# Kernel optimization log

Measured on AMD Instinct MI355X. Metric: run time of the kernel, lower is better.

The kernel has to match this reference:

```python
import jax, jax.numpy as jnp
import numpy as np

D_MODEL = 1024
NUM_EXPERTS = 16
TOP_K = 2
TOP_C = 4  # min(E, max(4, 2*top_k))
TAU = 1.0
RANK = 64  # max(4, d_model // 16)


def _stable_softmax(v):
    m = jnp.max(v, axis=-1, keepdims=True)
    e = jnp.exp(v - m)
    return e / (jnp.sum(e, axis=-1, keepdims=True) + 1e-12)


def setup_inputs() -> dict:
    key = jax.random.key(0)
    ks = jax.random.split(key, 8)
    B, D, E, R = 16384, D_MODEL, NUM_EXPERTS, RANK
    x = jax.random.normal(ks[0], (B, D), dtype=jnp.float32)
    W_enc = jax.random.normal(ks[1], (D, D), dtype=jnp.float32) * (1.0 / np.sqrt(D))
    b_enc = jnp.zeros((D,), dtype=jnp.float32)
    W_gate = jax.random.normal(ks[2], (E, D), dtype=jnp.float32) * (1.0 / np.sqrt(D))
    U = jax.random.normal(ks[3], (E, R, D), dtype=jnp.float32) * (1.0 / np.sqrt(D))
    V = jax.random.normal(ks[4], (E, D, R), dtype=jnp.float32) * (1.0 / np.sqrt(R))
    gamma = jnp.ones((E,), dtype=jnp.float32)
    return {"x": x, "W_enc": W_enc, "b_enc": b_enc, "W_gate": W_gate,
            "U": U, "V": V, "gamma": gamma}


def reference(x, W_enc, b_enc, W_gate, U, V, gamma):
    # shared encoder
    encoded = x @ W_enc.T + b_enc                      # [B, D]
    # gating: logits -> top_c -> top_k -> softmax over selected logits
    logits = (encoded @ W_gate.T) / TAU                # [B, E]
    topc_vals, topc_idx = jax.lax.top_k(logits, TOP_C)
    topk_vals, pos_in_c = jax.lax.top_k(topc_vals, TOP_K)
    topk_idx = jnp.take_along_axis(topc_idx, pos_in_c, axis=1)  # [B, K]
    topk_w = _stable_softmax(topk_vals)                # [B, K], all > 1e-12
    # dense per-(token, expert) combine weight (equivalent to gather/scatter)
    B = x.shape[0]
    w_dense = jnp.zeros((B, NUM_EXPERTS), dtype=x.dtype)
    w_dense = w_dense.at[jnp.arange(B)[:, None], topk_idx].add(topk_w)
    # low-rank experts: delta_e(x) = gamma_e * silu(x U_e^T) V_e^T
    s = jax.nn.silu(jnp.einsum('bd,erd->ber', encoded, U))        # [B, E, R]
    coef = w_dense * gamma[None, :]                               # [B, E]
    delta = jnp.einsum('ber,edr->bd', s * coef[..., None], V)     # [B, D]
    # y = encoded + sum_k w_k * (expert(x) - x)  with expert(x)-x = delta_e
    return encoded + delta
```

## Files before the change

kernel.cpp:

```cpp
#include <hip/hip_runtime.h>
#include <hip/hip_bf16.h>

#define D_DIM 1024
#define NE 16
#define RK 64
#define NTOK 16384

typedef __bf16 bf16;
typedef __bf16 bf16x8 __attribute__((ext_vector_type(8)));
typedef __bf16 bf16x4 __attribute__((ext_vector_type(4)));
typedef float f32x4 __attribute__((ext_vector_type(4)));

__device__ __forceinline__ void gload16(const void* g, void* l) {
  __builtin_amdgcn_global_load_lds((const __attribute__((address_space(1))) unsigned int*)g,
                                   (__attribute__((address_space(3))) unsigned int*)l,
                                   16, 0, 0);
}

__global__ void k_cast(const float* __restrict__ s, bf16* __restrict__ d, int n4) {
  int i = blockIdx.x * blockDim.x + threadIdx.x;
  if (i >= n4) return;
  float4 v = ((const float4*)s)[i];
  bf16x4 o = { (bf16)v.x, (bf16)v.y, (bf16)v.z, (bf16)v.w };
  ((bf16x4*)d)[i] = o;
}

__global__ void k_castv(const float* __restrict__ V, bf16* __restrict__ Vb2) {
  int id = blockIdx.x * 256 + threadIdx.x;
  int d = id & 1023;
  int rb = (id >> 10) & 7;
  int e = id >> 13;
  const float* src = V + ((size_t)(e * 1024 + d)) * 64 + rb * 8;
  float4 v0 = *(const float4*)src;
  float4 v1 = *(const float4*)(src + 4);
  bf16x8 o = { (bf16)v0.x, (bf16)v0.y, (bf16)v0.z, (bf16)v0.w,
               (bf16)v1.x, (bf16)v1.y, (bf16)v1.z, (bf16)v1.w };
  *(bf16x8*)(Vb2 + (size_t)id * 8) = o;
}

__global__ void k_gmat(const float* __restrict__ Wg, const float* __restrict__ We,
                       float* __restrict__ Gt2) {
  int d = blockIdx.x * 256 + threadIdx.x;
  int e = blockIdx.y;
  int j0 = blockIdx.z * 128;
  double a0 = 0.0, a1 = 0.0, a2 = 0.0, a3 = 0.0;
  for (int j = j0; j < j0 + 128; j += 4) {
    a0 += (double)Wg[e * D_DIM + j + 0] * (double)We[(size_t)(j + 0) * D_DIM + d];
    a1 += (double)Wg[e * D_DIM + j + 1] * (double)We[(size_t)(j + 1) * D_DIM + d];
    a2 += (double)Wg[e * D_DIM + j + 2] * (double)We[(size_t)(j + 2) * D_DIM + d];
    a3 += (double)Wg[e * D_DIM + j + 3] * (double)We[(size_t)(j + 3) * D_DIM + d];
  }
  atomicAdd(&Gt2[(d >> 2) * 64 + e * 4 + (d & 3)], (float)((a0 + a1) + (a2 + a3)));
}

__global__ void k_bgate(const float* __restrict__ Wg, const float* __restrict__ be,
                        float* __restrict__ bg) {
  __shared__ double red[256];
  int e = blockIdx.x, t = threadIdx.x;
  double a = 0.0;
  for (int j = t; j < D_DIM; j += 256) a += (double)Wg[e * D_DIM + j] * (double)be[j];
  red[t] = a; __syncthreads();
  for (int s = 128; s > 0; s >>= 1) { if (t < s) red[t] += red[t + s]; __syncthreads(); }
  if (t == 0) bg[e] = (float)red[0];
}

__global__ __launch_bounds__(256) void k_gatecast(const float* __restrict__ x,
                                                  const float* __restrict__ Gt2,
                                                  const float* __restrict__ bg,
                                                  const float* __restrict__ gamma,
                                                  bf16* __restrict__ xb,
                                                  int* __restrict__ pk,
                                                  float2* __restrict__ wpair) {
  __shared__ float bufx[8][1024];
  __shared__ float Ls[4 * 2 * NE];
  int tid = threadIdx.x;
  int wv = tid >> 6, lane = tid & 63;
  int g = lane & 15;
  int s = lane >> 4;
  int tokbase = blockIdx.x * 8 + wv * 2;

  const float* xr0 = x + (size_t)tokbase * D_DIM;
#pragma unroll
  for (int c = 0; c < 4; ++c) {
    gload16(xr0 + c * 256 + lane * 4, &bufx[wv * 2][c * 256 + lane * 4]);
    gload16(xr0 + D_DIM + c * 256 + lane * 4, &bufx[wv * 2 + 1][c * 256 + lane * 4]);
  }

  const float* Gq = Gt2 + s * 64 + g * 4;
  const float* b0p = &bufx[wv * 2][s * 4];
  const float* b1p = &bufx[wv * 2 + 1][s * 4];
  float acc0 = 0.0f, acc1 = 0.0f;
  float4 gv = *(const float4*)Gq;
  for (int it = 0; it < 64; ++it) {
    int nx = (it < 63) ? it + 1 : 0;
    float4 gn = *(const float4*)(Gq + (size_t)nx * 256);
    float4 x0 = *(const float4*)(b0p + it * 16);
    float4 x1 = *(const float4*)(b1p + it * 16);
    acc0 += x0.x * gv.x + x0.y * gv.y + x0.z * gv.z + x0.w * gv.w;
    acc1 += x1.x * gv.x + x1.y * gv.y + x1.z * gv.z + x1.w * gv.w;
    gv = gn;
  }
  acc0 += __shfl_xor(acc0, 16); acc0 += __shfl_xor(acc0, 32);
  acc1 += __shfl_xor(acc1, 16); acc1 += __shfl_xor(acc1, 32);
  if (s == 0) {
    Ls[wv * 32 + g] = acc0;
    Ls[wv * 32 + 16 + g] = acc1;
  }

#pragma unroll
  for (int t = 0; t < 2; ++t) {
    const float4* src = (const float4*)&bufx[wv * 2 + t][0];
    bf16x4* dst = (bf16x4*)(xb + (size_t)(tokbase + t) * D_DIM);
#pragma unroll
    for (int r = 0; r < 4; ++r) {
      float4 v = src[lane + 64 * r];
      bf16x4 o = { (bf16)v.x, (bf16)v.y, (bf16)v.z, (bf16)v.w };
      dst[lane + 64 * r] = o;
    }
  }
  __syncthreads();

  if (lane < 2) {
    int t = lane;
    int tok = tokbase + t;
    const float* lrow = &Ls[wv * 32 + t * 16];
    float v1 = -1e30f, v2 = -1e30f; int i1 = 0, i2 = 0;
#pragma unroll
    for (int e = 0; e < NE; ++e) {
      float v = lrow[e] + bg[e];
      if (v > v1) { v2 = v1; i2 = i1; v1 = v; i1 = e; }
      else if (v > v2) { v2 = v; i2 = e; }
    }
    float e1 = expf(v2 - v1);
    float den = 1.0f + e1 + 1e-12f;
    float w0 = (1.0f / den) * gamma[i1];
    float w1 = (e1 / den) * gamma[i2];
    pk[tok] = i1 | (i2 << 8);
    wpair[tok] = make_float2(w0, w1);
  }
}

__global__ __launch_bounds__(256) void k_scatter(const int* __restrict__ pk,
                                                 const float2* __restrict__ wpair,
                                                 int* __restrict__ cnt,
                                                 int* __restrict__ lists,
                                                 float* __restrict__ wl) {
  __shared__ int lc[32];
  __shared__ int base[32];
  __shared__ int lc2[32];
  int tid = threadIdx.x;
  int tok = blockIdx.x * 256 + tid;
  if (tid < 32) { lc[tid] = 0; lc2[tid] = 0; }
  __syncthreads();
  int p = pk[tok];
  float2 w = wpair[tok];
  int b0 = p & 0xff;
  int b1 = 16 + ((p >> 8) & 0xff);
  atomicAdd(&lc[b0], 1);
  atomicAdd(&lc[b1], 1);
  __syncthreads();
  if (tid < 32 && lc[tid] > 0) base[tid] = atomicAdd(&cnt[tid], lc[tid]);
  __syncthreads();
  int r0 = base[b0] + atomicAdd(&lc2[b0], 1);
  lists[(size_t)b0 * NTOK + r0] = tok;
  wl[(size_t)b0 * NTOK + r0] = w.x;
  int r1 = base[b1] + atomicAdd(&lc2[b1], 1);
  lists[(size_t)b1 * NTOK + r1] = tok;
  wl[(size_t)b1 * NTOK + r1] = w.y;
}

__global__ void k_btab(const int* __restrict__ cnt, int2* __restrict__ btab,
                       int* __restrict__ nblk) {
  int lane = threadIdx.x;
  int nb = (lane < 32) ? ((cnt[lane] + 63) >> 6) : 0;
  int pfx = nb;
  for (int off = 1; off < 32; off <<= 1) {
    int v = __shfl_up(pfx, off);
    if (lane >= off) pfx += v;
  }
  int start = pfx - nb;
  if (lane < 32) {
    int c = cnt[lane];
    int i = 0;
    for (int t0 = 0; t0 < c; t0 += 64, ++i)
      btab[start + i] = make_int2(lane, t0);
  }
  if (lane == 31) *nblk = pfx;
}

__global__ __launch_bounds__(512, 1) void k_encgemm(const bf16* __restrict__ A,
                                                    const bf16* __restrict__ W,
                                                    const float* __restrict__ bias,
                                                    bf16* __restrict__ encb) {
  __shared__ char smem[65536];
  bf16* const AsB = (bf16*)smem;
  bf16* const BsB = (bf16*)(smem + 32768);
  int tid = threadIdx.x;
  int w = blockIdx.x;
  int bm = (w & 63) * 256;
  int bn = (w >> 6) * 256;
  int lane = tid & 63, wv = tid >> 6;
  int wm = (wv >> 2) * 128, wn = (wv & 3) * 64;
  int srow = tid >> 2;
  int sc = (tid & 3) * 8;
  int fr = lane & 15, fk = (lane >> 4) * 8;
  f32x4 acc[8][4] = {};

  {
    bf16* as = AsB; bf16* bs = BsB;
    gload16(A + (size_t)(bm + srow) * D_DIM + sc, &as[srow * 32 + sc]);
    gload16(A + (size_t)(bm + 128 + srow) * D_DIM + sc, &as[(128 + srow) * 32 + sc]);
    gload16(W + (size_t)(bn + srow) * D_DIM + sc, &bs[srow * 32 + sc]);
    gload16(W + (size_t)(bn + 128 + srow) * D_DIM + sc, &bs[(128 + srow) * 32 + sc]);
  }
  __syncthreads();

  for (int k0 = 0; k0 < D_DIM; k0 += 32) {
    int cur = (k0 >> 5) & 1;
    if (k0 + 32 < D_DIM) {
      int kn = k0 + 32;
      bf16* as = AsB + (cur ^ 1) * 8192;
      bf16* bs = BsB + (cur ^ 1) * 8192;
      gload16(A + (size_t)(bm + srow) * D_DIM + kn + sc, &as[srow * 32 + sc]);
      gload16(A + (size_t)(bm + 128 + srow) * D_DIM + kn + sc, &as[(128 + srow) * 32 + sc]);
      gload16(W + (size_t)(bn + srow) * D_DIM + kn + sc, &bs[srow * 32 + sc]);
      gload16(W + (size_t)(bn + 128 + srow) * D_DIM + kn + sc, &bs[(128 + srow) * 32 + sc]);
    }
    const bf16* as = AsB + cur * 8192;
    const bf16* bs = BsB + cur * 8192;
    bf16x8 af[8], bv[4];
#pragma unroll
    for (int m = 0; m < 8; ++m)
      af[m] = *(const bf16x8*)&as[(wm + m * 16 + fr) * 32 + fk];
#pragma unroll
    for (int n = 0; n < 4; ++n)
      bv[n] = *(const bf16x8*)&bs[(wn + n * 16 + fr) * 32 + fk];
#pragma unroll
    for (int m = 0; m < 8; ++m)
#pragma unroll
      for (int n = 0; n < 4; ++n)
        acc[m][n] = __builtin_amdgcn_mfma_f32_16x16x32_bf16(af[m], bv[n], acc[m][n], 0, 0, 0);
    __syncthreads();
  }

  int rg = (lane >> 4) * 4;
  bf16* tb = (bf16*)smem + wv * 2176;
#pragma unroll
  for (int h = 0; h < 4; ++h) {
#pragma unroll
    for (int mi = 0; mi < 2; ++mi) {
      int m = h * 2 + mi;
#pragma unroll
      for (int n = 0; n < 4; ++n) {
        float bval = bias[bn + wn + n * 16 + fr];
#pragma unroll
        for (int r = 0; r < 4; ++r)
          tb[(mi * 16 + rg + r) * 68 + n * 16 + fr] = (bf16)(acc[m][n][r] + bval);
      }
    }
#pragma unroll
    for (int it2 = 0; it2 < 8; ++it2) {
      int row = it2 * 4 + (lane >> 4);
      int c4 = (lane & 15) * 4;
      *(ushort4*)&encb[(size_t)(bm + wm + h * 32 + row) * D_DIM + bn + wn + c4] =
        *(const ushort4*)&tb[row * 68 + c4];
    }
  }
}

__global__ __launch_bounds__(256) void k_expert(const bf16* __restrict__ encb,
                                                const bf16* __restrict__ Ub,
                                                const bf16* __restrict__ Vb2,
                                                const int* __restrict__ cnt,
                                                const int* __restrict__ lists,
                                                const float* __restrict__ wl,
                                                const int2* __restrict__ btab,
                                                const int* __restrict__ nblk,
                                                bf16* __restrict__ d0,
                                                bf16* __restrict__ d1) {
  int bid = blockIdx.x;
  if (bid >= *nblk) return;
  int2 bt = btab[bid];
  int bin = bt.x, t0 = bt.y;
  int slot = bin >> 4, e = bin & 15;
  int c = cnt[bin];
  int nrows = c - t0; if (nrows > 64) nrows = 64;
  const int* tl = lists + (size_t)bin * NTOK + t0;
  const float* wlp = wl + (size_t)bin * NTOK + t0;

  __shared__ int toks[64];
  __shared__ float coefs[64];
  __shared__ bf16 As[2][64 * 64];
  __shared__ bf16 Us[2][64 * 64];
  __shared__ bf16 Ss[64 * 64];
  __shared__ bf16 xtrb[4][64 * 34];

  int tid = threadIdx.x;
  if (tid < 64) {
    int rr = tid < nrows ? tid : nrows - 1;
    toks[tid] = tl[rr];
    coefs[tid] = tid < nrows ? wlp[tid] : 0.0f;
  }
  __syncthreads();

  int lane = tid & 63, wv = tid >> 6;
  int srow = tid >> 3;
  int sc8 = tid & 7;
  int cs = (sc8 ^ (srow & 7)) * 8;
  int scol = sc8 * 8;
  int fr = lane & 15, fk = (lane >> 4) * 8;
  size_t tokA0 = (size_t)toks[srow] * D_DIM;
  size_t tokA1 = (size_t)toks[32 + srow] * D_DIM;
  const bf16* Ue = Ub + (size_t)e * RK * D_DIM;
  f32x4 acc1[4] = {};

  gload16(encb + tokA0 + cs, &As[0][srow * 64 + scol]);
  gload16(encb + tokA1 + cs, &As[0][(32 + srow) * 64 + scol]);
  gload16(Ue + (size_t)srow * D_DIM + cs, &Us[0][srow * 64 + scol]);
  gload16(Ue + (size_t)(32 + srow) * D_DIM + cs, &Us[0][(32 + srow) * 64 + scol]);
  __syncthreads();

  for (int k0 = 0; k0 < D_DIM; k0 += 64) {
    int cur = (k0 >> 6) & 1;
    if (k0 + 64 < D_DIM) {
      int kn = k0 + 64;
      gload16(encb + tokA0 + kn + cs, &As[cur ^ 1][srow * 64 + scol]);
      gload16(encb + tokA1 + kn + cs, &As[cur ^ 1][(32 + srow) * 64 + scol]);
      gload16(Ue + (size_t)srow * D_DIM + kn + cs, &Us[cur ^ 1][srow * 64 + scol]);
      gload16(Ue + (size_t)(32 + srow) * D_DIM + kn + cs, &Us[cur ^ 1][(32 + srow) * 64 + scol]);
    }
    int arow = wv * 16 + fr;
    int sw = (fr & 7) << 3;
#pragma unroll
    for (int kk = 0; kk < 2; ++kk) {
      bf16x8 af = *(const bf16x8*)&As[cur][(arow * 64 + kk * 32 + fk) ^ sw];
#pragma unroll
      for (int n = 0; n < 4; ++n) {
        bf16x8 bv = *(const bf16x8*)&Us[cur][((n * 16 + fr) * 64 + kk * 32 + fk) ^ sw];
        acc1[n] = __builtin_amdgcn_mfma_f32_16x16x32_bf16(af, bv, acc1[n], 0, 0, 0);
      }
    }
    __syncthreads();
  }

  int rg = (lane >> 4) * 4;
#pragma unroll
  for (int n = 0; n < 4; ++n)
#pragma unroll
    for (int r = 0; r < 4; ++r) {
      int row = wv * 16 + rg + r;
      float v = acc1[n][r];
      float s = v / (1.0f + __expf(-v));
      Ss[row * 64 + n * 16 + fr] = (bf16)(s * coefs[row]);
    }
  __syncthreads();
  bf16x8 a2[4][2];
#pragma unroll
  for (int m = 0; m < 4; ++m)
#pragma unroll
    for (int kk = 0; kk < 2; ++kk)
      a2[m][kk] = *(const bf16x8*)&Ss[(m * 16 + fr) * 64 + kk * 32 + fk];

  const bf16* Ve2 = Vb2 + (size_t)e * RK * D_DIM;
  bf16* dst = slot ? d1 : d0;
  int rb0 = lane >> 4;
  int colbase = wv * 256;
  bf16* tb = xtrb[wv];
  for (int njb = 0; njb < 8; ++njb) {
#pragma unroll
    for (int nj2 = 0; nj2 < 2; ++nj2) {
      int nj = njb * 2 + nj2;
      int dcol = colbase + nj * 16 + fr;
      bf16x8 b0 = *(const bf16x8*)&Ve2[((size_t)rb0 * D_DIM + dcol) * 8];
      bf16x8 b1 = *(const bf16x8*)&Ve2[((size_t)(rb0 + 4) * D_DIM + dcol) * 8];
#pragma unroll
      for (int m = 0; m < 4; ++m) {
        f32x4 a = {};
        a = __builtin_amdgcn_mfma_f32_16x16x32_bf16(a2[m][0], b0, a, 0, 0, 0);
        a = __builtin_amdgcn_mfma_f32_16x16x32_bf16(a2[m][1], b1, a, 0, 0, 0);
#pragma unroll
        for (int r = 0; r < 4; ++r)
          tb[(m * 16 + rg + r) * 34 + nj2 * 16 + fr] = (bf16)a[r];
      }
    }
#pragma unroll
    for (int it2 = 0; it2 < 16; ++it2) {
      int row = it2 * 4 + (lane >> 4);
      int c2 = (lane & 15) * 2;
      if (row < nrows)
        *(ushort2*)&dst[(size_t)toks[row] * D_DIM + colbase + njb * 32 + c2] =
          *(const ushort2*)&tb[row * 34 + c2];
    }
  }
}

__global__ __launch_bounds__(256) void k_final(float* __restrict__ out,
                                               const bf16* __restrict__ encb,
                                               const bf16* __restrict__ d0,
                                               const bf16* __restrict__ d1) {
  size_t i = ((size_t)blockIdx.x * 256 + threadIdx.x) * 8;
  bf16x8 e = *(const bf16x8*)(encb + i);
  bf16x8 a = *(const bf16x8*)(d0 + i);
  bf16x8 b = *(const bf16x8*)(d1 + i);
  float4 o0, o1;
  o0.x = (float)e[0] + (float)a[0] + (float)b[0];
  o0.y = (float)e[1] + (float)a[1] + (float)b[1];
  o0.z = (float)e[2] + (float)a[2] + (float)b[2];
  o0.w = (float)e[3] + (float)a[3] + (float)b[3];
  o1.x = (float)e[4] + (float)a[4] + (float)b[4];
  o1.y = (float)e[5] + (float)a[5] + (float)b[5];
  o1.z = (float)e[6] + (float)a[6] + (float)b[6];
  o1.w = (float)e[7] + (float)a[7] + (float)b[7];
  *(float4*)(out + i) = o0;
  *(float4*)(out + i + 4) = o1;
}

extern "C" void kernel_launch(void* const* d_in, const int* in_sizes, int n_in,
                              void* d_out, int out_size, void* d_ws, size_t ws_size,
                              hipStream_t stream) {
  const float* x   = (const float*)d_in[0];
  const float* We  = (const float*)d_in[1];
  const float* be  = (const float*)d_in[2];
  const float* Wg  = (const float*)d_in[3];
  const float* U   = (const float*)d_in[4];
  const float* V   = (const float*)d_in[5];
  const float* gam = (const float*)d_in[6];
  float* out = (float*)d_out;
  char* ws = (char*)d_ws;

  int*    cnt  = (int*)(ws + 0);
  float*  Gt2  = (float*)(ws + 256);
  float*  bg   = (float*)(ws + 66048);
  int2*   btab = (int2*)(ws + 66176);
  int*    nblk = (int*)(ws + 70656);
  bf16*   xb   = (bf16*)(ws + 131072);
  bf16*   d0   = (bf16*)(ws + 131072);
  bf16*   encb = (bf16*)(ws + 131072 + 33554432);
  char*   base = ws + 131072 + 2 * 33554432;
  bf16*   Wb   = (bf16*)(base);
  bf16*   Ubf  = (bf16*)(base + 2097152);
  bf16*   Vb2  = (bf16*)(base + 2 * 2097152);
  int*    lists= (int*)(base + 3 * 2097152);
  float*  wl   = (float*)(base + 4 * 2097152);
  int*    pk   = (int*)(base + 5 * 2097152);
  float2* wpr  = (float2*)(base + 5 * 2097152 + 131072);
  bf16*   d1   = (bf16*)(base + 5 * 2097152 + 131072 + 131072 + 131072);

  hipMemsetAsync(ws, 0, 66048, stream);

  k_cast<<<1024, 256, 0, stream>>>(We, Wb, 1048576 / 4);
  k_cast<<<1024, 256, 0, stream>>>(U, Ubf, 1048576 / 4);
  k_castv<<<512, 256, 0, stream>>>(V, Vb2);

  dim3 gg(4, 16, 8);
  k_gmat<<<gg, 256, 0, stream>>>(Wg, We, Gt2);
  k_bgate<<<16, 256, 0, stream>>>(Wg, be, bg);

  k_gatecast<<<2048, 256, 0, stream>>>(x, Gt2, bg, gam, xb, pk, wpr);
  k_scatter<<<64, 256, 0, stream>>>(pk, wpr, cnt, lists, wl);
  k_btab<<<1, 64, 0, stream>>>(cnt, btab, nblk);

  k_encgemm<<<256, 512, 0, stream>>>(xb, Wb, be, encb);

  k_expert<<<544, 256, 0, stream>>>(encb, Ubf, Vb2, cnt, lists, wl, btab, nblk, d0, d1);
  k_final<<<8192, 256, 0, stream>>>(out, encb, d0, d1);
}
```

Baseline: 193.7 us.

## Shrink expert kernel LDS by single-buffering and aliasing transpose buffer

Replaces the double-buffered A/U LDS tiles with a single buffer and aliases the per-wave output transpose scratch onto that same buffer. This roughly halves shared memory per block so more blocks fit per CU. It also XOR-swizzles the S tile to avoid bank conflicts and drops the padding from the transpose stride. In exchange, global loads no longer overlap the MFMA work, adding a barrier per k-step, and the unpadded transpose stride may cause bank conflicts.

```diff
diff --git a/kernel.cpp b/kernel.cpp
--- a/kernel.cpp
+++ b/kernel.cpp
@@ -290,10 +290,10 @@
 
   __shared__ int toks[64];
   __shared__ float coefs[64];
-  __shared__ bf16 As[2][64 * 64];
-  __shared__ bf16 Us[2][64 * 64];
+  __shared__ bf16 AU[8192];
   __shared__ bf16 Ss[64 * 64];
-  __shared__ bf16 xtrb[4][64 * 34];
+  bf16* const As = AU;
+  bf16* const Us = AU + 4096;
 
   int tid = threadIdx.x;
   if (tid < 64) {
@@ -306,43 +306,32 @@
   int lane = tid & 63, wv = tid >> 6;
   int srow = tid >> 3;
   int sc8 = tid & 7;
+  int scol = sc8 * 8;
   int cs = (sc8 ^ (srow & 7)) * 8;
-  int scol = sc8 * 8;
   int fr = lane & 15, fk = (lane >> 4) * 8;
+  int sw = (fr & 7) << 3;
   size_t tokA0 = (size_t)toks[srow] * D_DIM;
   size_t tokA1 = (size_t)toks[32 + srow] * D_DIM;
   const bf16* Ue = Ub + (size_t)e * RK * D_DIM;
   f32x4 acc1[4] = {};
 
-  gload16(encb + tokA0 + cs, &As[0][srow * 64 + scol]);
-  gload16(encb + tokA1 + cs, &As[0][(32 + srow) * 64 + scol]);
-  gload16(Ue + (size_t)srow * D_DIM + cs, &Us[0][srow * 64 + scol]);
-  gload16(Ue + (size_t)(32 + srow) * D_DIM + cs, &Us[0][(32 + srow) * 64 + scol]);
-  __syncthreads();
-
   for (int k0 = 0; k0 < D_DIM; k0 += 64) {
-    int cur = (k0 >> 6) & 1;
-    if (k0 + 64 < D_DIM) {
-      int kn = k0 + 64;
-      gload16(encb + tokA0 + kn + cs, &As[cur ^ 1][srow * 64 + scol]);
-      gload16(encb + tokA1 + kn + cs, &As[cur ^ 1][(32 + srow) * 64 + scol]);
-      gload16(Ue + (size_t)srow * D_DIM + kn + cs, &Us[cur ^ 1][srow * 64 + scol]);
-      gload16(Ue + (size_t)(32 + srow) * D_DIM + kn + cs, &Us[cur ^ 1][(32 + srow) * 64 + scol]);
-    }
-    int arow = wv * 16 + fr;
-    int sw = (fr & 7) << 3;
+    __syncthreads();
+    gload16(encb + tokA0 + k0 + cs, &As[srow * 64 + scol]);
+    gload16(encb + tokA1 + k0 + cs, &As[(32 + srow) * 64 + scol]);
+    gload16(Ue + (size_t)srow * D_DIM + k0 + cs, &Us[srow * 64 + scol]);
+    gload16(Ue + (size_t)(32 + srow) * D_DIM + k0 + cs, &Us[(32 + srow) * 64 + scol]);
+    __syncthreads();
 #pragma unroll
     for (int kk = 0; kk < 2; ++kk) {
-      bf16x8 af = *(const bf16x8*)&As[cur][(arow * 64 + kk * 32 + fk) ^ sw];
+      bf16x8 af = *(const bf16x8*)&As[((wv * 16 + fr) * 64 + kk * 32 + fk) ^ sw];
 #pragma unroll
       for (int n = 0; n < 4; ++n) {
-        bf16x8 bv = *(const bf16x8*)&Us[cur][((n * 16 + fr) * 64 + kk * 32 + fk) ^ sw];
+        bf16x8 bv = *(const bf16x8*)&Us[((n * 16 + fr) * 64 + kk * 32 + fk) ^ sw];
         acc1[n] = __builtin_amdgcn_mfma_f32_16x16x32_bf16(af, bv, acc1[n], 0, 0, 0);
       }
     }
-    __syncthreads();
-  }
-
+  }
   int rg = (lane >> 4) * 4;
 #pragma unroll
   for (int n = 0; n < 4; ++n)
@@ -351,7 +340,7 @@
       int row = wv * 16 + rg + r;
       float v = acc1[n][r];
       float s = v / (1.0f + __expf(-v));
-      Ss[row * 64 + n * 16 + fr] = (bf16)(s * coefs[row]);
+      Ss[(row * 64 + n * 16 + fr) ^ (((rg + r) & 7) << 3)] = (bf16)(s * coefs[row]);
     }
   __syncthreads();
   bf16x8 a2[4][2];
@@ -359,13 +348,14 @@
   for (int m = 0; m < 4; ++m)
 #pragma unroll
     for (int kk = 0; kk < 2; ++kk)
-      a2[m][kk] = *(const bf16x8*)&Ss[(m * 16 + fr) * 64 + kk * 32 + fk];
+      a2[m][kk] = *(const bf16x8*)&Ss[((m * 16 + fr) * 64 + kk * 32 + fk) ^ sw];
+  __syncthreads();
 
   const bf16* Ve2 = Vb2 + (size_t)e * RK * D_DIM;
   bf16* dst = slot ? d1 : d0;
   int rb0 = lane >> 4;
   int colbase = wv * 256;
-  bf16* tb = xtrb[wv];
+  bf16* tb = AU + wv * 2048;
   for (int njb = 0; njb < 8; ++njb) {
 #pragma unroll
     for (int nj2 = 0; nj2 < 2; ++nj2) {
@@ -380,7 +370,7 @@
         a = __builtin_amdgcn_mfma_f32_16x16x32_bf16(a2[m][1], b1, a, 0, 0, 0);
 #pragma unroll
         for (int r = 0; r < 4; ++r)
-          tb[(m * 16 + rg + r) * 34 + nj2 * 16 + fr] = (bf16)a[r];
+          tb[(m * 16 + rg + r) * 32 + nj2 * 16 + fr] = (bf16)a[r];
       }
     }
 #pragma unroll
@@ -389,7 +379,7 @@
       int c2 = (lane & 15) * 2;
       if (row < nrows)
         *(ushort2*)&dst[(size_t)toks[row] * D_DIM + colbase + njb * 32 + c2] =
-          *(const ushort2*)&tb[row * 34 + c2];
+          *(const ushort2*)&tb[row * 32 + c2];
     }
   }
 }
```

Result: faster. 163.4 us (-15.6%).
